# Optimization experiments

Hardware: AMD Instinct MI355X
Metric: run time of the kernel (lower is better)

Reference implementation:

```python
import jax, jax.numpy as jnp
import numpy as np
from jax import lax

BOX_STRIDES = (32, 64, 128, 256)
MASK_STRIDE = 4
MASK_SIZE = 28
PATCH = 512
TOPK = 64
SCORE_TH = 0.5
IOU_TH = 0.5
MASK_TH = 0.5


def setup_inputs():
    key = jax.random.key(0)
    ks = jax.random.split(key, 10)
    d = {}
    d["pred0"] = jax.random.normal(ks[0], (2, 6, 16, 16), jnp.float32)
    d["pred1"] = jax.random.normal(ks[1], (2, 6, 8, 8), jnp.float32)
    d["pred2"] = jax.random.normal(ks[2], (2, 6, 4, 4), jnp.float32)
    d["pred3"] = jax.random.normal(ks[3], (2, 6, 2, 2), jnp.float32)
    d["feat0"] = jax.random.normal(ks[4], (2, 64, 128, 128), jnp.float32)
    d["feat1"] = jax.random.normal(ks[5], (2, 64, 64, 64), jnp.float32)
    d["feat2"] = jax.random.normal(ks[6], (2, 64, 32, 32), jnp.float32)
    d["feat3"] = jax.random.normal(ks[7], (2, 64, 16, 16), jnp.float32)
    d["w1"] = jax.random.normal(ks[8], (128, 256, 3, 3), jnp.float32) * 0.05
    d["b1"] = jnp.zeros((128,), jnp.float32)
    d["w2"] = jax.random.normal(ks[9], (1, 128, 1, 1), jnp.float32) * 0.05
    d["b2"] = jnp.zeros((1,), jnp.float32)
    return d


def _decode_level(pred, stride):
    # pred: [B, 6, H, W] -> [B, H*W, 6], (cx,cy)=(p+grid)*stride, wh=exp(p)*stride
    B, no, H, W = pred.shape
    p = pred.transpose(0, 2, 3, 1).reshape(B, H * W, no)
    gy, gx = jnp.meshgrid(jnp.arange(H), jnp.arange(W), indexing="ij")
    grid = jnp.stack([gx.ravel(), gy.ravel()], axis=-1).astype(p.dtype)  # [HW,2] (x,y)
    xy = (p[..., 0:2] + grid) * stride
    wh = jnp.exp(p[..., 2:4]) * stride
    return jnp.concatenate([xy, wh, p[..., 4:]], axis=-1)


def _iou_matrix(b):
    # b: [K,4] xyxy
    area = jnp.clip(b[:, 2] - b[:, 0], 0) * jnp.clip(b[:, 3] - b[:, 1], 0)
    ix0 = jnp.maximum(b[:, None, 0], b[None, :, 0])
    iy0 = jnp.maximum(b[:, None, 1], b[None, :, 1])
    ix1 = jnp.minimum(b[:, None, 2], b[None, :, 2])
    iy1 = jnp.minimum(b[:, None, 3], b[None, :, 3])
    inter = jnp.clip(ix1 - ix0, 0) * jnp.clip(iy1 - iy0, 0)
    union = area[:, None] + area[None, :] - inter
    return inter / jnp.maximum(union, 1e-9)


def _nms_keep(boxes, labels, valid):
    # boxes already sorted by descending score; batched NMS via per-class coord offset
    off = labels.astype(boxes.dtype)[:, None] * (PATCH * 8.0)
    iou = _iou_matrix(boxes + off)
    idx = jnp.arange(TOPK)

    def body(i, keep):
        sup = keep[i] & (iou[i] > IOU_TH) & (idx > i)
        return keep & ~sup

    return lax.fori_loop(0, TOPK, body, valid)


def _roi_align_one(feat, box):
    # feat: [C,Hf,Wf]; box: [4] xyxy in image coords (spatial_scale=1/MASK_STRIDE)
    # torchvision-style aligned=False, one bilinear sample per bin center
    C, Hf, Wf = feat.shape
    b = box / MASK_STRIDE
    bw = (b[2] - b[0]) / MASK_SIZE
    bh = (b[3] - b[1]) / MASK_SIZE
    xs = b[0] + (jnp.arange(MASK_SIZE, dtype=feat.dtype) + 0.5) * bw
    ys = b[1] + (jnp.arange(MASK_SIZE, dtype=feat.dtype) + 0.5) * bh
    x = jnp.clip(jnp.broadcast_to(xs[None, :], (MASK_SIZE, MASK_SIZE)), 0.0, Wf - 1.0)
    y = jnp.clip(jnp.broadcast_to(ys[:, None], (MASK_SIZE, MASK_SIZE)), 0.0, Hf - 1.0)
    x0 = jnp.floor(x).astype(jnp.int32)
    y0 = jnp.floor(y).astype(jnp.int32)
    x1 = jnp.minimum(x0 + 1, Wf - 1)
    y1 = jnp.minimum(y0 + 1, Hf - 1)
    fx = x - x0
    fy = y - y0
    v00 = feat[:, y0, x0]
    v01 = feat[:, y0, x1]
    v10 = feat[:, y1, x0]
    v11 = feat[:, y1, x1]
    return (v00 * (1 - fy) * (1 - fx) + v01 * (1 - fy) * fx
            + v10 * fy * (1 - fx) + v11 * fy * fx)  # [C,S,S]


def _paste_one(mask_soft, box_int):
    # nearest-neighbor upsample of [S,S] mask into its box on a [P,P] canvas
    x0, y0, x1, y1 = box_int[0], box_int[1], box_int[2], box_int[3]
    h = y1 - y0 + 1
    w = x1 - x0 + 1
    ys = jnp.arange(PATCH, dtype=jnp.int32)
    xs = jnp.arange(PATCH, dtype=jnp.int32)
    iy = jnp.clip((ys - y0) * MASK_SIZE // h, 0, MASK_SIZE - 1)
    ix = jnp.clip((xs - x0) * MASK_SIZE // w, 0, MASK_SIZE - 1)
    g = mask_soft[iy][:, ix]  # [P,P]
    inside = ((ys >= y0) & (ys <= y1))[:, None] & ((xs >= x0) & (xs <= x1))[None, :]
    return jnp.where(inside, g, 0.0)


def _conv(x, w, b, pad):
    y = lax.conv_general_dilated(x, w, (1, 1), pad, dimension_numbers=("NCHW", "OIHW", "NCHW"))
    return y + b[None, :, None, None]


def _pipeline(pred0, pred1, pred2, pred3, feat0, feat1, feat2, feat3, w1, b1, w2, b2):
    # box branch: decode per-level predictions
    yolo = jnp.concatenate(
        [_decode_level(p, s) for p, s in zip([pred0, pred1, pred2, pred3], BOX_STRIDES)],
        axis=1,
    )  # [B,N,6]
    B = yolo.shape[0]
    cx, cy, w_, h_ = yolo[..., 0], yolo[..., 1], yolo[..., 2], yolo[..., 3]
    boxes = jnp.stack([cx - w_ / 2, cy - h_ / 2, cx + w_ / 2, cy + h_ / 2], axis=-1)
    scores = jax.nn.sigmoid(yolo[..., 4])
    labels = jnp.argmax(yolo[..., 5:], axis=-1)
    valid = scores > SCORE_TH
    top_scores, top_idx = lax.top_k(jnp.where(valid, scores, 0.0), TOPK)
    boxes_k = jnp.take_along_axis(boxes, top_idx[..., None], axis=1)  # [B,K,4]
    labels_k = jnp.take_along_axis(labels, top_idx, axis=1)
    valid_k = top_scores > SCORE_TH
    keep = jax.vmap(_nms_keep)(boxes_k, labels_k, valid_k)  # [B,K] bool

    # mask branch: merge mask feats at the first level's resolution (nearest)
    H0, W0 = feat0.shape[2], feat0.shape[3]
    merged = jnp.concatenate(
        [feat0] + [jax.image.resize(f, (B, f.shape[1], H0, W0), "nearest") for f in [feat1, feat2, feat3]],
        axis=1,
    )  # [B,256,H0,W0]
    rois = jax.vmap(lambda f, bx: jax.vmap(lambda bb: _roi_align_one(f, bb))(bx))(merged, boxes_k)
    C = rois.shape[2]
    x = rois.reshape(B * TOPK, C, MASK_SIZE, MASK_SIZE)
    hdn = jax.nn.silu(_conv(x, w1, b1, "SAME"))
    logits = _conv(hdn, w2, b2, "SAME")  # [B*K,1,S,S]
    soft = jax.nn.sigmoid(logits).reshape(B, TOPK, MASK_SIZE, MASK_SIZE)

    box_int = jnp.clip(boxes_k, 0, PATCH - 1).astype(jnp.int32)
    pasted = jax.vmap(jax.vmap(_paste_one))(soft, box_int)  # [B,K,P,P]
    return top_scores, boxes_k, labels_k, pasted, keep


def reference(pred0, pred1, pred2, pred3, feat0, feat1, feat2, feat3, w1, b1, w2, b2):
    top_scores, boxes_k, labels_k, pasted, keep = _pipeline(
        pred0, pred1, pred2, pred3, feat0, feat1, feat2, feat3, w1, b1, w2, b2
    )
    out_scores = top_scores * keep
    bin_masks = (pasted > MASK_TH) & keep[:, :, None, None]
    return out_scores, boxes_k, labels_k.astype(jnp.int32), bin_masks, keep
```

## Files before the change

### kernel.cpp

```cpp
#include <hip/hip_runtime.h>
#include <hip/hip_bf16.h>
#include <cstdint>

#define NTOPK 64
#define A_TOT 340
#define MS 28

#define OFF_SCORES 0
#define OFF_BOXES  128
#define OFF_LABELS 640
#define OFF_MASKS  768
#define OFF_KEEP   33555200ull

typedef __attribute__((ext_vector_type(8))) short bf16x8;
typedef __attribute__((ext_vector_type(4))) float f32x4;

__device__ __forceinline__ float sigmoidf_(float x) { return 1.f / (1.f + expf(-x)); }
__device__ __forceinline__ float bf2f(unsigned u) {
  return __uint_as_float(u << 16);
}
__device__ __forceinline__ unsigned short f2bf(float f) {
  __hip_bfloat16 h = __float2bfloat16(f);
  return *(unsigned short*)&h;
}

__global__ __launch_bounds__(256) void k_prep(
    const float* __restrict__ p0, const float* __restrict__ p1,
    const float* __restrict__ p2, const float* __restrict__ p3,
    const float* __restrict__ f0, const float* __restrict__ f1,
    const float* __restrict__ f2, const float* __restrict__ f3,
    const float* __restrict__ w1,
    float* __restrict__ out,
    float* __restrict__ ws_boxes, int* __restrict__ ws_keep,
    int* __restrict__ ws_boxint,
    unsigned short* __restrict__ wt, unsigned short* __restrict__ mg)
{
  __shared__ __align__(16) char smem_raw[128 * 260 * 2];
  const int bid = blockIdx.x;
  const int t = threadIdx.x;

  if (bid < 2) {
    const int b = bid;
    float* sc = (float*)smem_raw;
    float(*bx)[4] = (float(*)[4])(sc + A_TOT);
    float* tk_score = (float*)(bx + A_TOT);
    float(*tk_box)[4] = (float(*)[4])(tk_score + 64);

    for (int a = t; a < A_TOT; a += 256) {
      const float* pp; int W, HW, la; float stride;
      if (a < 256)      { pp = p0; W = 16; HW = 256; la = a;       stride = 32.f;  }
      else if (a < 320) { pp = p1; W = 8;  HW = 64;  la = a - 256; stride = 64.f;  }
      else if (a < 336) { pp = p2; W = 4;  HW = 16;  la = a - 320; stride = 128.f; }
      else              { pp = p3; W = 2;  HW = 4;   la = a - 336; stride = 256.f; }
      const float* base = pp + (size_t)b * 6 * HW + la;
      float v0 = base[0], v1 = base[HW], v2 = base[2 * HW], v3 = base[3 * HW], v4 = base[4 * HW];
      int gx = la % W, gy = la / W;
      float cx = (v0 + (float)gx) * stride;
      float cy = (v1 + (float)gy) * stride;
      float w_ = expf(v2) * stride;
      float h_ = expf(v3) * stride;
      float score = sigmoidf_(v4);
      sc[a] = (score > 0.5f) ? score : 0.f;
      bx[a][0] = cx - 0.5f * w_;
      bx[a][1] = cy - 0.5f * h_;
      bx[a][2] = cx + 0.5f * w_;
      bx[a][3] = cy + 0.5f * h_;
    }
    __syncthreads();

    for (int a = t; a < A_TOT; a += 256) {
      float my = sc[a];
      int rank = 0;
      for (int j = 0; j < A_TOT; ++j) {
        float o = sc[j];
        rank += (o > my) || (o == my && j < a);
      }
      if (rank < NTOPK) {
        tk_score[rank] = my;
        tk_box[rank][0] = bx[a][0];
        tk_box[rank][1] = bx[a][1];
        tk_box[rank][2] = bx[a][2];
        tk_box[rank][3] = bx[a][3];
      }
    }
    __syncthreads();

    if (t < NTOPK) {
      float x0 = tk_box[t][0], y0 = tk_box[t][1];
      float x1 = tk_box[t][2], y1 = tk_box[t][3];
      float s = tk_score[t];
      float area = fmaxf(x1 - x0, 0.f) * fmaxf(y1 - y0, 0.f);
      int keep = (s > 0.5f) ? 1 : 0;
      for (int i = 0; i < NTOPK - 1; ++i) {
        int   ki = __shfl(keep, i);
        float a0 = __shfl(x0, i);
        float c0 = __shfl(y0, i);
        float a1 = __shfl(x1, i);
        float c1 = __shfl(y1, i);
        float ai = __shfl(area, i);
        if (ki && t > i && keep) {
          float ix0 = fmaxf(a0, x0), iy0 = fmaxf(c0, y0);
          float ix1 = fminf(a1, x1), iy1 = fminf(c1, y1);
          float inter = fmaxf(ix1 - ix0, 0.f) * fmaxf(iy1 - iy0, 0.f);
          float uni = ai + area - inter;
          float iou = inter / fmaxf(uni, 1e-9f);
          if (iou > 0.5f) keep = 0;
        }
      }
      int box = b * NTOPK + t;
      out[OFF_SCORES + box] = keep ? s : 0.f;
      float bv[4] = {x0, y0, x1, y1};
      #pragma unroll
      for (int c = 0; c < 4; ++c) {
        out[OFF_BOXES + box * 4 + c] = bv[c];
        ws_boxes[box * 4 + c] = bv[c];
        float bc = fminf(fmaxf(bv[c], 0.f), 511.f);
        ws_boxint[box * 4 + c] = (int)bc;
      }
      out[OFF_LABELS + box] = 0.f;
      out[OFF_KEEP + box] = keep ? 1.f : 0.f;
      ws_keep[box] = keep;
    }
    return;
  }

  if (bid < 130) {
    const int co = bid - 2;
    const int ci = t;
    const int c = ci >> 5, cil = ci & 31;
    const int cq = co >> 5, col = co & 31;
    const float* src = w1 + ((size_t)co * 256 + ci) * 9;
    #pragma unroll
    for (int tap = 0; tap < 9; ++tap)
      wt[(((size_t)(cq * 8 + c) * 9 + tap)) * 1024 + col * 32 + cil] = f2bf(src[tap]);
    return;
  }

  {
    const int idx = bid - 130;
    const int b = idx >> 7;
    const int y = idx & 127;
    unsigned short* tile = (unsigned short*)smem_raw;
    const int x = t & 127, ch = t >> 7;

    {
      const float* src = f0 + ((size_t)b * 64) * 16384 + y * 128 + x;
      for (int cc = 0; cc < 32; ++cc) {
        int cl = ch * 32 + cc;
        tile[x * 260 + cl] = f2bf(src[(size_t)cl * 16384]);
      }
    }
    {
      const float* src = f1 + ((size_t)b * 64) * 4096 + (y >> 1) * 64 + (x >> 1);
      for (int cc = 0; cc < 32; ++cc) {
        int cl = ch * 32 + cc;
        tile[x * 260 + 64 + cl] = f2bf(src[(size_t)cl * 4096]);
      }
    }
    {
      const float* src = f2 + ((size_t)b * 64) * 1024 + (y >> 2) * 32 + (x >> 2);
      for (int cc = 0; cc < 32; ++cc) {
        int cl = ch * 32 + cc;
        tile[x * 260 + 128 + cl] = f2bf(src[(size_t)cl * 1024]);
      }
    }
    {
      const float* src = f3 + ((size_t)b * 64) * 256 + (y >> 3) * 16 + (x >> 3);
      for (int cc = 0; cc < 32; ++cc) {
        int cl = ch * 32 + cc;
        tile[x * 260 + 192 + cl] = f2bf(src[(size_t)cl * 256]);
      }
    }
    __syncthreads();
    unsigned short* dst = mg + (((size_t)b * 128 + y) * 128) * 256;
    for (int it = 0; it < 32; ++it) {
      int qq = t + it * 256;
      int xx = qq >> 6, cg = qq & 63;
      *(ushort4*)(dst + xx * 256 + cg * 4) = *(ushort4*)&tile[xx * 260 + cg * 4];
    }
  }
}

__global__ __launch_bounds__(256) void k_roistage(
    const unsigned short* __restrict__ mg,
    const float* __restrict__ ws_boxes, const int* __restrict__ ws_keep,
    unsigned short* __restrict__ roi)
{
  const int boxLo = blockIdx.x & 7;
  const int r2 = blockIdx.x >> 3;
  const int r = r2 % 30;
  const int box = ((r2 / 30) << 3) | boxLo;
  if (!ws_keep[box]) return;
  const int t = threadIdx.x;
  unsigned short* rbox = roi + (size_t)box * 8 * 30 * 1024;
  const int gr = r - 1;

  if (gr < 0 || gr > 27) {
    uint4 z = {0u, 0u, 0u, 0u};
    for (int e = t; e < 1024; e += 256) {
      int chunk = e >> 7, rem = e & 127;
      size_t off = ((size_t)(chunk * 30 + r)) * 1024 + rem * 8;
      *(uint4*)(rbox + off) = z;
    }
    return;
  }

  __shared__ int   xa_s[MS], xb_s[MS];
  __shared__ float fx_s[MS];
  __shared__ float by_s[4];
  if (t < 4) by_s[t] = ws_boxes[box * 4 + t];
  __syncthreads();
  const float b0 = by_s[0] * 0.25f, b1_ = by_s[1] * 0.25f;
  const float b2_ = by_s[2] * 0.25f, b3_ = by_s[3] * 0.25f;
  if (t < MS) {
    float bw = (b2_ - b0) * (1.f / MS);
    float x = b0 + ((float)t + 0.5f) * bw;
    x = fminf(fmaxf(x, 0.f), 127.f);
    int x0 = (int)floorf(x);
    xa_s[t] = x0; xb_s[t] = min(x0 + 1, 127); fx_s[t] = x - (float)x0;
  }
  float bh = (b3_ - b1_) * (1.f / MS);
  float yy = b1_ + ((float)gr + 0.5f) * bh;
  yy = fminf(fmaxf(yy, 0.f), 127.f);
  int ya = (int)floorf(yy);
  int yb = min(ya + 1, 127);
  float fy = yy - (float)ya;
  __syncthreads();

  const int b = box >> 6;
  const unsigned short* mgb = mg + ((size_t)b * 128 * 128) * 256;

  for (int e = t; e < 1024; e += 256) {
    int chunk = e >> 7, rem = e & 127;
    int cell = rem >> 2, quad = rem & 3;
    size_t off = ((size_t)(chunk * 30 + r)) * 1024 + rem * 8;
    int gc = cell - 1;
    if (gc < 0 || gc > 27) {
      uint4 z = {0u, 0u, 0u, 0u};
      *(uint4*)(rbox + off) = z;
      continue;
    }
    int U = chunk * 4 + quad;
    int xa = xa_s[gc], xb = xb_s[gc];
    float fx = fx_s[gc];
    float w00 = (1.f - fy) * (1.f - fx), w01 = (1.f - fy) * fx;
    float w10 = fy * (1.f - fx),         w11 = fy * fx;
    uint4 A = *(const uint4*)(mgb + ((size_t)(ya * 128 + xa)) * 256 + U * 8);
    uint4 B = *(const uint4*)(mgb + ((size_t)(ya * 128 + xb)) * 256 + U * 8);
    uint4 C = *(const uint4*)(mgb + ((size_t)(yb * 128 + xa)) * 256 + U * 8);
    uint4 D = *(const uint4*)(mgb + ((size_t)(yb * 128 + xb)) * 256 + U * 8);
    const unsigned* pa = (const unsigned*)&A;
    const unsigned* pb = (const unsigned*)&B;
    const unsigned* pc = (const unsigned*)&C;
    const unsigned* pd = (const unsigned*)&D;
    unsigned o[4];
    #pragma unroll
    for (int k2 = 0; k2 < 4; ++k2) {
      float lo = bf2f(pa[k2] & 0xffffu) * w00 + bf2f(pb[k2] & 0xffffu) * w01 +
                 bf2f(pc[k2] & 0xffffu) * w10 + bf2f(pd[k2] & 0xffffu) * w11;
      float hi = bf2f(pa[k2] >> 16) * w00 + bf2f(pb[k2] >> 16) * w01 +
                 bf2f(pc[k2] >> 16) * w10 + bf2f(pd[k2] >> 16) * w11;
      o[k2] = (unsigned)f2bf(lo) | ((unsigned)f2bf(hi) << 16);
    }
    uint4 pk; pk.x = o[0]; pk.y = o[1]; pk.z = o[2]; pk.w = o[3];
    *(uint4*)(rbox + off) = pk;
  }
}

__global__ __launch_bounds__(256, 4) void k_conv(
    const unsigned short* __restrict__ roi,
    const unsigned short* __restrict__ wt,
    const float* __restrict__ b1, const float* __restrict__ w2,
    const int* __restrict__ ws_keep,
    float* __restrict__ ws_logit4)
{
  const int bid = blockIdx.x;
  const int boxLo = bid & 7;
  const int r1 = bid >> 3;
  const int cq = r1 & 3;
  const int q = (r1 >> 2) & 3;
  const int box = ((r1 >> 4) << 3) | boxLo;
  if (!ws_keep[box]) return;
  const int t = threadIdx.x;
  const int lane = t & 63, wv = t >> 6;
  const int laneN = lane & 15, kg = lane >> 4;

  __shared__ __align__(16) unsigned short ldsA[9216];
  __shared__ __align__(16) unsigned short ldsB[9216];

  int badd[4][3];
  bool act[4];
  #pragma unroll
  for (int i = 0; i < 4; ++i) {
    int tile = wv * 4 + i;
    act[i] = (tile * 16) < 196;
    int p = tile * 16 + laneN;
    if (p > 195) p = 195;
    int py = p / 28, px = p - py * 28;
    #pragma unroll
    for (int dx = 0; dx < 3; ++dx) {
      int cell = px + dx;
      badd[i][dx] = (py * 32 + cell) * 32 + (kg ^ ((cell >> 1) & 3)) * 8;
    }
  }

  f32x4 acc[2][4];
  #pragma unroll
  for (int m = 0; m < 2; ++m)
    #pragma unroll
    for (int i = 0; i < 4; ++i) acc[m][i] = (f32x4){0.f, 0.f, 0.f, 0.f};

  const uint4* rbase = (const uint4*)roi;
  const uint4* wbase = (const uint4*)wt;

  uint4 ga0, ga1, ga2, ga3, ga4;
  uint4 gb0, gb1, gb2, gb3, gb4;
  auto issue_load = [&](int c) {
    const uint4* wa = wbase + (size_t)(cq * 8 + c) * 1152;
    ga0 = wa[t]; ga1 = wa[t + 256]; ga2 = wa[t + 512]; ga3 = wa[t + 768];
    if (t < 128) ga4 = wa[t + 1024];
    const uint4* s = rbase + ((size_t)(box * 8 + c) * 30 + q * 7) * 128;
    gb0 = s[t]; gb1 = s[t + 256]; gb2 = s[t + 512]; gb3 = s[t + 768];
    if (t < 128) gb4 = s[t + 1024];
  };

  issue_load(0);
  #pragma unroll 1
  for (int c = 0; c < 8; ++c) {
    {
      uint4* da = (uint4*)ldsA;
      da[t] = ga0; da[t + 256] = ga1; da[t + 512] = ga2; da[t + 768] = ga3;
      if (t < 128) da[t + 1024] = ga4;
      auto put = [&](int e, uint4 v) {
        int r = e >> 7, rem = e & 127;
        int cell = rem >> 2, qd = rem & 3;
        *(uint4*)(ldsB + (r * 128 + cell * 4 + (qd ^ ((cell >> 1) & 3))) * 8) = v;
      };
      put(t, gb0); put(t + 256, gb1); put(t + 512, gb2); put(t + 768, gb3);
      if (t < 128) put(t + 1024, gb4);
    }
    __syncthreads();
    if (c < 7) issue_load(c + 1);
    #pragma unroll
    for (int tap = 0; tap < 9; ++tap) {
      const int dy = tap / 3, dx = tap % 3;
      bf16x8 av0 = *(const bf16x8*)(ldsA + tap * 1024 + laneN * 32 + kg * 8);
      bf16x8 av1 = *(const bf16x8*)(ldsA + tap * 1024 + 512 + laneN * 32 + kg * 8);
      #pragma unroll
      for (int i = 0; i < 4; ++i) {
        if (act[i]) {
          bf16x8 bv = *(const bf16x8*)(ldsB + badd[i][dx] + dy * 1024);
          acc[0][i] = __builtin_amdgcn_mfma_f32_16x16x32_bf16(av0, bv, acc[0][i], 0, 0, 0);
          acc[1][i] = __builtin_amdgcn_mfma_f32_16x16x32_bf16(av1, bv, acc[1][i], 0, 0, 0);
        }
      }
    }
    __syncthreads();
  }

  float b1v[2][4], w2v[2][4];
  #pragma unroll
  for (int m = 0; m < 2; ++m)
    #pragma unroll
    for (int r = 0; r < 4; ++r) {
      int co = cq * 32 + m * 16 + kg * 4 + r;
      b1v[m][r] = b1[co];
      w2v[m][r] = w2[co];
    }
  #pragma unroll
  for (int i = 0; i < 4; ++i) {
    if (!act[i]) continue;
    float part = 0.f;
    #pragma unroll
    for (int m = 0; m < 2; ++m)
      #pragma unroll
      for (int r = 0; r < 4; ++r) {
        float h = acc[m][i][r] + b1v[m][r];
        part = fmaf(w2v[m][r], h * sigmoidf_(h), part);
      }
    part += __shfl_xor(part, 16);
    part += __shfl_xor(part, 32);
    int p = (wv * 4 + i) * 16 + laneN;
    if (kg == 0 && p < 196)
      ws_logit4[((size_t)box * 4 + cq) * 784 + q * 196 + p] = part;
  }
}

__global__ __launch_bounds__(256) void k_paste(
    const float* __restrict__ ws_logit4, const int* __restrict__ ws_keep,
    const int* __restrict__ ws_boxint, const float* __restrict__ b2,
    float* __restrict__ out)
{
  const int box = blockIdx.x >> 4;
  const int yo  = blockIdx.x & 15;
  const int t = threadIdx.x;
  float* mb = out + OFF_MASKS + (size_t)box * 262144 + (size_t)yo * 32 * 512;

  if (!ws_keep[box]) {
    f32x4 z = {0.f, 0.f, 0.f, 0.f};
    f32x4* p = (f32x4*)mb;
    for (int e = t; e < 4096; e += 256)
      __builtin_nontemporal_store(z, p + e);
    return;
  }

  __shared__ float soft[784];
  __shared__ int iys[32];
  __shared__ int bi[4];
  if (t < 4) bi[t] = ws_boxint[box * 4 + t];
  __syncthreads();
  const int x0 = bi[0], y0 = bi[1], x1 = bi[2], y1 = bi[3];
  const int w = x1 - x0 + 1, h = y1 - y0 + 1;
  const float b2v = b2[0];
  const float* l0 = ws_logit4 + (size_t)box * 4 * 784;

  for (int e = t; e < 784; e += 256)
    soft[e] = sigmoidf_(l0[e] + l0[784 + e] + l0[1568 + e] + l0[2352 + e] + b2v);
  if (t < 32) {
    int Y = yo * 32 + t;
    int vy = (Y - y0) * MS;
    int iy = (vy >= 0) ? (vy / h) : 0;
    iys[t] = min(max(iy, 0), MS - 1);
  }
  __syncthreads();

  const int c4 = (t & 127) * 4;
  const int rr = t >> 7;
  int ixr[4];
  bool inx[4];
  #pragma unroll
  for (int u = 0; u < 4; ++u) {
    int X = c4 + u;
    int vx = (X - x0) * MS;
    int ix = (vx >= 0) ? (vx / w) : 0;
    ixr[u] = min(max(ix, 0), MS - 1);
    inx[u] = (X >= x0) && (X <= x1);
  }

  int prev_iy = -1;
  f32x4 v = {0.f, 0.f, 0.f, 0.f};
  #pragma unroll 1
  for (int it = 0; it < 16; ++it) {
    int Yl = it * 2 + rr;
    int Y = yo * 32 + Yl;
    f32x4 o;
    if (Y >= y0 && Y <= y1) {
      int iy = iys[Yl];
      if (iy != prev_iy) {
        prev_iy = iy;
        #pragma unroll
        for (int u = 0; u < 4; ++u)
          v[u] = (inx[u] && soft[iy * MS + ixr[u]] > 0.5f) ? 1.f : 0.f;
      }
      o = v;
    } else {
      o = (f32x4){0.f, 0.f, 0.f, 0.f};
    }
    __builtin_nontemporal_store(o, (f32x4*)(mb + (size_t)Yl * 512 + c4));
  }
}

extern "C" void kernel_launch(void* const* d_in, const int* in_sizes, int n_in,
                              void* d_out, int out_size, void* d_ws, size_t ws_size,
                              hipStream_t stream) {
  const float* p0 = (const float*)d_in[0];
  const float* p1 = (const float*)d_in[1];
  const float* p2 = (const float*)d_in[2];
  const float* p3 = (const float*)d_in[3];
  const float* f0 = (const float*)d_in[4];
  const float* f1 = (const float*)d_in[5];
  const float* f2 = (const float*)d_in[6];
  const float* f3 = (const float*)d_in[7];
  const float* w1 = (const float*)d_in[8];
  const float* b1 = (const float*)d_in[9];
  const float* w2 = (const float*)d_in[10];
  const float* b2 = (const float*)d_in[11];
  float* out = (float*)d_out;

  float* wsf = (float*)d_ws;
  float*          ws_boxes  = wsf;
  int*            ws_keep   = (int*)(wsf + 512);
  int*            ws_boxint = (int*)(wsf + 640);
  float*          ws_logit4 = wsf + 1152;
  unsigned short* ws_wt     = (unsigned short*)(wsf + 402560);
  unsigned short* ws_merged = (unsigned short*)(wsf + 550016);
  unsigned short* ws_roi    = (unsigned short*)(wsf + 4744320);

  k_prep<<<386, 256, 0, stream>>>(p0, p1, p2, p3, f0, f1, f2, f3, w1,
                                  out, ws_boxes, ws_keep, ws_boxint,
                                  ws_wt, ws_merged);
  k_roistage<<<3840, 256, 0, stream>>>(ws_merged, ws_boxes, ws_keep, ws_roi);
  k_conv<<<2048, 256, 0, stream>>>(ws_roi, ws_wt, b1, w2, ws_keep, ws_logit4);
  k_paste<<<2048, 256, 0, stream>>>(ws_logit4, ws_keep, ws_boxint, b2, out);
}
```

Before: 283.1 us.

## Load conv weights directly to registers and double-buffer ROI tiles in LDS

The conv kernel no longer stages weights through shared memory. Each lane loads its own weight fragments for all nine taps straight from global memory into registers. The ROI input tile is now double-buffered in LDS, which removes the second barrier per channel chunk. The XOR swizzle on the ROI layout is dropped, and launch bounds are lowered from 4 to 3 blocks per CU to leave room for the extra registers. The risks are higher register pressure, possible LDS bank conflicts without the swizzle, and uncoalesced per-lane weight loads.

```diff
diff --git a/kernel.cpp b/kernel.cpp
--- a/kernel.cpp
+++ b/kernel.cpp
@@ -267,7 +267,7 @@
   }
 }
 
-__global__ __launch_bounds__(256, 4) void k_conv(
+__global__ __launch_bounds__(256, 3) void k_conv(
     const unsigned short* __restrict__ roi,
     const unsigned short* __restrict__ wt,
     const float* __restrict__ b1, const float* __restrict__ w2,
@@ -285,8 +285,7 @@
   const int lane = t & 63, wv = t >> 6;
   const int laneN = lane & 15, kg = lane >> 4;
 
-  __shared__ __align__(16) unsigned short ldsA[9216];
-  __shared__ __align__(16) unsigned short ldsB[9216];
+  __shared__ __align__(16) unsigned short ldsB[2][9216];
 
   int badd[4][3];
   bool act[4];
@@ -298,10 +297,8 @@
     if (p > 195) p = 195;
     int py = p / 28, px = p - py * 28;
     #pragma unroll
-    for (int dx = 0; dx < 3; ++dx) {
-      int cell = px + dx;
-      badd[i][dx] = (py * 32 + cell) * 32 + (kg ^ ((cell >> 1) & 3)) * 8;
-    }
+    for (int dx = 0; dx < 3; ++dx)
+      badd[i][dx] = (py * 32 + px + dx) * 32 + kg * 8;
   }
 
   f32x4 acc[2][4];
@@ -311,51 +308,49 @@
     for (int i = 0; i < 4; ++i) acc[m][i] = (f32x4){0.f, 0.f, 0.f, 0.f};
 
   const uint4* rbase = (const uint4*)roi;
-  const uint4* wbase = (const uint4*)wt;
-
-  uint4 ga0, ga1, ga2, ga3, ga4;
+  const bf16x8* wtl = (const bf16x8*)wt;
+
   uint4 gb0, gb1, gb2, gb3, gb4;
-  auto issue_load = [&](int c) {
-    const uint4* wa = wbase + (size_t)(cq * 8 + c) * 1152;
-    ga0 = wa[t]; ga1 = wa[t + 256]; ga2 = wa[t + 512]; ga3 = wa[t + 768];
-    if (t < 128) ga4 = wa[t + 1024];
+  auto prefB = [&](int c) {
     const uint4* s = rbase + ((size_t)(box * 8 + c) * 30 + q * 7) * 128;
     gb0 = s[t]; gb1 = s[t + 256]; gb2 = s[t + 512]; gb3 = s[t + 768];
     if (t < 128) gb4 = s[t + 1024];
   };
-
-  issue_load(0);
+  auto storeB = [&](int buf) {
+    uint4* d = (uint4*)ldsB[buf];
+    d[t] = gb0; d[t + 256] = gb1; d[t + 512] = gb2; d[t + 768] = gb3;
+    if (t < 128) d[t + 1024] = gb4;
+  };
+
+  prefB(0);
+  storeB(0);
   #pragma unroll 1
   for (int c = 0; c < 8; ++c) {
+    bf16x8 A0[9], A1[9];
     {
-      uint4* da = (uint4*)ldsA;
-      da[t] = ga0; da[t + 256] = ga1; da[t + 512] = ga2; da[t + 768] = ga3;
-      if (t < 128) da[t + 1024] = ga4;
-      auto put = [&](int e, uint4 v) {
-        int r = e >> 7, rem = e & 127;
-        int cell = rem >> 2, qd = rem & 3;
-        *(uint4*)(ldsB + (r * 128 + cell * 4 + (qd ^ ((cell >> 1) & 3))) * 8) = v;
-      };
-      put(t, gb0); put(t + 256, gb1); put(t + 512, gb2); put(t + 768, gb3);
-      if (t < 128) put(t + 1024, gb4);
+      const bf16x8* wa = wtl + (size_t)(cq * 8 + c) * 1152;
+      #pragma unroll
+      for (int tap = 0; tap < 9; ++tap) {
+        A0[tap] = wa[tap * 128 + laneN * 4 + kg];
+        A1[tap] = wa[tap * 128 + 64 + laneN * 4 + kg];
+      }
     }
     __syncthreads();
-    if (c < 7) issue_load(c + 1);
+    if (c < 7) prefB(c + 1);
+    const unsigned short* rb = ldsB[c & 1];
     #pragma unroll
     for (int tap = 0; tap < 9; ++tap) {
       const int dy = tap / 3, dx = tap % 3;
-      bf16x8 av0 = *(const bf16x8*)(ldsA + tap * 1024 + laneN * 32 + kg * 8);
-      bf16x8 av1 = *(const bf16x8*)(ldsA + tap * 1024 + 512 + laneN * 32 + kg * 8);
       #pragma unroll
       for (int i = 0; i < 4; ++i) {
         if (act[i]) {
-          bf16x8 bv = *(const bf16x8*)(ldsB + badd[i][dx] + dy * 1024);
-          acc[0][i] = __builtin_amdgcn_mfma_f32_16x16x32_bf16(av0, bv, acc[0][i], 0, 0, 0);
-          acc[1][i] = __builtin_amdgcn_mfma_f32_16x16x32_bf16(av1, bv, acc[1][i], 0, 0, 0);
+          bf16x8 bv = *(const bf16x8*)(rb + badd[i][dx] + dy * 1024);
+          acc[0][i] = __builtin_amdgcn_mfma_f32_16x16x32_bf16(A0[tap], bv, acc[0][i], 0, 0, 0);
+          acc[1][i] = __builtin_amdgcn_mfma_f32_16x16x32_bf16(A1[tap], bv, acc[1][i], 0, 0, 0);
         }
       }
     }
-    __syncthreads();
+    if (c < 7) storeB((c + 1) & 1);
   }
 
   float b1v[2][4], w2v[2][4];
```

Result: slower. 304.6 us (+7.6%).

## Switch mask-head conv to FP8 MFMA with swizzled fp8 weight and ROI layouts

Applied to the files above, without the earlier changes.

Converts the 3x3 conv weights and the ROI-aligned features to FP8 (e4m3) instead of bf16, and runs the conv with 16x16x32 fp8 MFMA. This halves the bytes loaded per channel chunk and the LDS footprint. The LDS bank swizzle moves from the staging stores into the global layouts, so tiles are copied into LDS with plain vector stores. The cost is much lower precision in the conv, which could flip thresholded mask bits near 0.5.

```diff
diff --git a/kernel.cpp b/kernel.cpp
--- a/kernel.cpp
+++ b/kernel.cpp
@@ -12,8 +12,8 @@
 #define OFF_MASKS  768
 #define OFF_KEEP   33555200ull
 
-typedef __attribute__((ext_vector_type(8))) short bf16x8;
 typedef __attribute__((ext_vector_type(4))) float f32x4;
+typedef long fp8x8;
 
 __device__ __forceinline__ float sigmoidf_(float x) { return 1.f / (1.f + expf(-x)); }
 __device__ __forceinline__ float bf2f(unsigned u) {
@@ -33,7 +33,7 @@
     float* __restrict__ out,
     float* __restrict__ ws_boxes, int* __restrict__ ws_keep,
     int* __restrict__ ws_boxint,
-    unsigned short* __restrict__ wt, unsigned short* __restrict__ mg)
+    unsigned char* __restrict__ wt, unsigned short* __restrict__ mg)
 {
   __shared__ __align__(16) char smem_raw[128 * 260 * 2];
   const int bid = blockIdx.x;
@@ -129,10 +129,14 @@
     const int ci = t;
     const int c = ci >> 5, cil = ci & 31;
     const int cq = co >> 5, col = co & 31;
+    const int slot = ((cil >> 3) ^ ((col >> 2) & 3)) * 8 + (cil & 7);
     const float* src = w1 + ((size_t)co * 256 + ci) * 9;
     #pragma unroll
-    for (int tap = 0; tap < 9; ++tap)
-      wt[(((size_t)(cq * 8 + c) * 9 + tap)) * 1024 + col * 32 + cil] = f2bf(src[tap]);
+    for (int tap = 0; tap < 9; ++tap) {
+      unsigned u = __builtin_amdgcn_cvt_pk_fp8_f32(src[tap], 0.f, 0, false);
+      wt[(((size_t)(cq * 8 + c) * 9 + tap)) * 1024 + col * 32 + slot] =
+          (unsigned char)(u & 0xff);
+    }
     return;
   }
 
@@ -184,7 +188,7 @@
 __global__ __launch_bounds__(256) void k_roistage(
     const unsigned short* __restrict__ mg,
     const float* __restrict__ ws_boxes, const int* __restrict__ ws_keep,
-    unsigned short* __restrict__ roi)
+    unsigned char* __restrict__ roi)
 {
   const int boxLo = blockIdx.x & 7;
   const int r2 = blockIdx.x >> 3;
@@ -192,15 +196,17 @@
   const int box = ((r2 / 30) << 3) | boxLo;
   if (!ws_keep[box]) return;
   const int t = threadIdx.x;
-  unsigned short* rbox = roi + (size_t)box * 8 * 30 * 1024;
+  unsigned char* rbox = roi + (size_t)box * 8 * 30 * 1024;
   const int gr = r - 1;
 
   if (gr < 0 || gr > 27) {
-    uint4 z = {0u, 0u, 0u, 0u};
+    uint2 z = {0u, 0u};
     for (int e = t; e < 1024; e += 256) {
       int chunk = e >> 7, rem = e & 127;
-      size_t off = ((size_t)(chunk * 30 + r)) * 1024 + rem * 8;
-      *(uint4*)(rbox + off) = z;
+      int cell = rem >> 2, quad = rem & 3;
+      size_t off = ((size_t)(chunk * 30 + r)) * 1024 + cell * 32 +
+                   (quad ^ ((cell >> 2) & 3)) * 8;
+      *(uint2*)(rbox + off) = z;
     }
     return;
   }
@@ -233,11 +239,12 @@
   for (int e = t; e < 1024; e += 256) {
     int chunk = e >> 7, rem = e & 127;
     int cell = rem >> 2, quad = rem & 3;
-    size_t off = ((size_t)(chunk * 30 + r)) * 1024 + rem * 8;
+    size_t off = ((size_t)(chunk * 30 + r)) * 1024 + cell * 32 +
+                 (quad ^ ((cell >> 2) & 3)) * 8;
     int gc = cell - 1;
     if (gc < 0 || gc > 27) {
-      uint4 z = {0u, 0u, 0u, 0u};
-      *(uint4*)(rbox + off) = z;
+      uint2 z = {0u, 0u};
+      *(uint2*)(rbox + off) = z;
       continue;
     }
     int U = chunk * 4 + quad;
@@ -253,23 +260,26 @@
     const unsigned* pb = (const unsigned*)&B;
     const unsigned* pc = (const unsigned*)&C;
     const unsigned* pd = (const unsigned*)&D;
-    unsigned o[4];
+    float f[8];
     #pragma unroll
     for (int k2 = 0; k2 < 4; ++k2) {
-      float lo = bf2f(pa[k2] & 0xffffu) * w00 + bf2f(pb[k2] & 0xffffu) * w01 +
-                 bf2f(pc[k2] & 0xffffu) * w10 + bf2f(pd[k2] & 0xffffu) * w11;
-      float hi = bf2f(pa[k2] >> 16) * w00 + bf2f(pb[k2] >> 16) * w01 +
-                 bf2f(pc[k2] >> 16) * w10 + bf2f(pd[k2] >> 16) * w11;
-      o[k2] = (unsigned)f2bf(lo) | ((unsigned)f2bf(hi) << 16);
-    }
-    uint4 pk; pk.x = o[0]; pk.y = o[1]; pk.z = o[2]; pk.w = o[3];
-    *(uint4*)(rbox + off) = pk;
+      f[2 * k2] = bf2f(pa[k2] & 0xffffu) * w00 + bf2f(pb[k2] & 0xffffu) * w01 +
+                  bf2f(pc[k2] & 0xffffu) * w10 + bf2f(pd[k2] & 0xffffu) * w11;
+      f[2 * k2 + 1] = bf2f(pa[k2] >> 16) * w00 + bf2f(pb[k2] >> 16) * w01 +
+                      bf2f(pc[k2] >> 16) * w10 + bf2f(pd[k2] >> 16) * w11;
+    }
+    unsigned o0 = __builtin_amdgcn_cvt_pk_fp8_f32(f[0], f[1], 0, false);
+    o0 = __builtin_amdgcn_cvt_pk_fp8_f32(f[2], f[3], o0, true);
+    unsigned o1 = __builtin_amdgcn_cvt_pk_fp8_f32(f[4], f[5], 0, false);
+    o1 = __builtin_amdgcn_cvt_pk_fp8_f32(f[6], f[7], o1, true);
+    uint2 pk; pk.x = o0; pk.y = o1;
+    *(uint2*)(rbox + off) = pk;
   }
 }
 
 __global__ __launch_bounds__(256, 4) void k_conv(
-    const unsigned short* __restrict__ roi,
-    const unsigned short* __restrict__ wt,
+    const unsigned char* __restrict__ roi,
+    const unsigned char* __restrict__ wt,
     const float* __restrict__ b1, const float* __restrict__ w2,
     const int* __restrict__ ws_keep,
     float* __restrict__ ws_logit4)
@@ -285,8 +295,7 @@
   const int lane = t & 63, wv = t >> 6;
   const int laneN = lane & 15, kg = lane >> 4;
 
-  __shared__ __align__(16) unsigned short ldsA[9216];
-  __shared__ __align__(16) unsigned short ldsB[9216];
+  __shared__ __align__(16) unsigned char lds[18432];
 
   int badd[4][3];
   bool act[4];
@@ -300,9 +309,10 @@
     #pragma unroll
     for (int dx = 0; dx < 3; ++dx) {
       int cell = px + dx;
-      badd[i][dx] = (py * 32 + cell) * 32 + (kg ^ ((cell >> 1) & 3)) * 8;
-    }
-  }
+      badd[i][dx] = 9216 + py * 1024 + cell * 32 + (kg ^ ((cell >> 2) & 3)) * 8;
+    }
+  }
+  const int aswz = (kg ^ ((laneN >> 2) & 3)) * 8;
 
   f32x4 acc[2][4];
   #pragma unroll
@@ -313,45 +323,41 @@
   const uint4* rbase = (const uint4*)roi;
   const uint4* wbase = (const uint4*)wt;
 
-  uint4 ga0, ga1, ga2, ga3, ga4;
-  uint4 gb0, gb1, gb2, gb3, gb4;
+  uint4 ga0, ga1, ga2;
+  uint4 gb0, gb1, gb2;
   auto issue_load = [&](int c) {
-    const uint4* wa = wbase + (size_t)(cq * 8 + c) * 1152;
-    ga0 = wa[t]; ga1 = wa[t + 256]; ga2 = wa[t + 512]; ga3 = wa[t + 768];
-    if (t < 128) ga4 = wa[t + 1024];
-    const uint4* s = rbase + ((size_t)(box * 8 + c) * 30 + q * 7) * 128;
-    gb0 = s[t]; gb1 = s[t + 256]; gb2 = s[t + 512]; gb3 = s[t + 768];
-    if (t < 128) gb4 = s[t + 1024];
+    const uint4* wa = wbase + (size_t)(cq * 8 + c) * 576;
+    ga0 = wa[t]; ga1 = wa[t + 256];
+    if (t < 64) ga2 = wa[t + 512];
+    const uint4* s = rbase + ((size_t)(box * 8 + c) * 30 + q * 7) * 64;
+    gb0 = s[t]; gb1 = s[t + 256];
+    if (t < 64) gb2 = s[t + 512];
   };
 
   issue_load(0);
   #pragma unroll 1
   for (int c = 0; c < 8; ++c) {
     {
-      uint4* da = (uint4*)ldsA;
-      da[t] = ga0; da[t + 256] = ga1; da[t + 512] = ga2; da[t + 768] = ga3;
-      if (t < 128) da[t + 1024] = ga4;
-      auto put = [&](int e, uint4 v) {
-        int r = e >> 7, rem = e & 127;
-        int cell = rem >> 2, qd = rem & 3;
-        *(uint4*)(ldsB + (r * 128 + cell * 4 + (qd ^ ((cell >> 1) & 3))) * 8) = v;
-      };
-      put(t, gb0); put(t + 256, gb1); put(t + 512, gb2); put(t + 768, gb3);
-      if (t < 128) put(t + 1024, gb4);
+      uint4* da = (uint4*)lds;
+      da[t] = ga0; da[t + 256] = ga1;
+      if (t < 64) da[t + 512] = ga2;
+      uint4* db = (uint4*)(lds + 9216);
+      db[t] = gb0; db[t + 256] = gb1;
+      if (t < 64) db[t + 512] = gb2;
     }
     __syncthreads();
     if (c < 7) issue_load(c + 1);
     #pragma unroll
     for (int tap = 0; tap < 9; ++tap) {
       const int dy = tap / 3, dx = tap % 3;
-      bf16x8 av0 = *(const bf16x8*)(ldsA + tap * 1024 + laneN * 32 + kg * 8);
-      bf16x8 av1 = *(const bf16x8*)(ldsA + tap * 1024 + 512 + laneN * 32 + kg * 8);
+      fp8x8 av0 = *(const fp8x8*)(lds + tap * 1024 + laneN * 32 + aswz);
+      fp8x8 av1 = *(const fp8x8*)(lds + tap * 1024 + 512 + laneN * 32 + aswz);
       #pragma unroll
       for (int i = 0; i < 4; ++i) {
         if (act[i]) {
-          bf16x8 bv = *(const bf16x8*)(ldsB + badd[i][dx] + dy * 1024);
-          acc[0][i] = __builtin_amdgcn_mfma_f32_16x16x32_bf16(av0, bv, acc[0][i], 0, 0, 0);
-          acc[1][i] = __builtin_amdgcn_mfma_f32_16x16x32_bf16(av1, bv, acc[1][i], 0, 0, 0);
+          fp8x8 bv = *(const fp8x8*)(lds + badd[i][dx] + dy * 1024);
+          acc[0][i] = __builtin_amdgcn_mfma_f32_16x16x32_fp8_fp8(av0, bv, acc[0][i], 0, 0, 0);
+          acc[1][i] = __builtin_amdgcn_mfma_f32_16x16x32_fp8_fp8(av1, bv, acc[1][i], 0, 0, 0);
         }
       }
     }
@@ -482,9 +488,9 @@
   int*            ws_keep   = (int*)(wsf + 512);
   int*            ws_boxint = (int*)(wsf + 640);
   float*          ws_logit4 = wsf + 1152;
-  unsigned short* ws_wt     = (unsigned short*)(wsf + 402560);
-  unsigned short* ws_merged = (unsigned short*)(wsf + 550016);
-  unsigned short* ws_roi    = (unsigned short*)(wsf + 4744320);
+  unsigned char*  ws_wt     = (unsigned char*)(wsf + 402560);
+  unsigned short* ws_merged = (unsigned short*)(wsf + 476288);
+  unsigned char*  ws_roi    = (unsigned char*)(wsf + 4670592);
 
   k_prep<<<386, 256, 0, stream>>>(p0, p1, p2, p3, f0, f1, f2, f3, w1,
                                   out, ws_boxes, ws_keep, ws_boxint,
```

New measurement: 263.1 us (median of 2 runs). 1.08x faster.
